# Kernel tuning notes

Measured on AMD Instinct MI355X. Metric: run time of the kernel, lower is better.

Reference implementation:

```python
import jax, jax.numpy as jnp
import numpy as np

Q_PTS = jnp.array([0.0, 0.25, 0.5, 0.75, 1.0], dtype=jnp.float32)
LN_EPS = 1e-5


def _lower_median(s):
    # torch.median returns the LOWER of the two middle values for even n
    return s[..., (s.shape[-1] - 1) // 2]


def _quantile_sorted(s, q):
    # torch.quantile default 'linear' interpolation, computed on pre-sorted s
    n = s.shape[-1]
    idx = q * (n - 1)
    lo = jnp.floor(idx).astype(jnp.int32)
    hi = jnp.ceil(idx).astype(jnp.int32)
    frac = (idx - lo).astype(s.dtype)
    return jnp.take(s, lo, axis=-1) * (1.0 - frac) + jnp.take(s, hi, axis=-1) * frac


def _robust_stats(flat):
    # flat: [L-1, B, N] -> [L-1, B, 7]  (median, MAD, 5 quantiles)
    s = jnp.sort(flat, axis=-1)
    med = _lower_median(s)[..., None]
    mad = _lower_median(jnp.sort(jnp.abs(flat - med), axis=-1))[..., None]
    q = _quantile_sorted(s, Q_PTS)
    return jnp.concatenate([med, mad, q], axis=-1)


def _layer_norm(x, eps=LN_EPS):
    mu = x.mean(-1, keepdims=True)
    var = ((x - mu) ** 2).mean(-1, keepdims=True)
    return (x - mu) * jax.lax.rsqrt(var + eps)


def _forward(ws, bs, fc1_w, fc1_b, ln_w, ln_b, gate_w, gate_b, fco_w, fco_b, scale):
    Lm1, B = ws.shape[0], ws.shape[1]
    w_flat = ws.reshape(Lm1, B, -1)
    b_flat = bs.reshape(Lm1, B, -1)
    w_feats = _robust_stats(w_flat)            # [L-1, B, 7]
    b_feats = _robust_stats(b_flat)            # [L-1, B, 7]
    g_mean = w_flat.mean(-1, keepdims=True)    # [L-1, B, 1]
    g_mad = jnp.zeros_like(g_mean)             # MAD over a size-1 axis is exactly 0
    combined = jnp.concatenate([w_feats, b_feats, g_mean, g_mad], axis=-1)  # [L-1, B, 16]
    x = _layer_norm(combined)                  # F.layer_norm without affine
    # ResidualMLP (vectorized over the layer axis l)
    h = jnp.einsum('lbi,lhi->lbh', x, fc1_w) + fc1_b[:, None, :]
    h = _layer_norm(h) * ln_w[:, None, :] + ln_b[:, None, :]
    h = jax.nn.gelu(h, approximate=False)      # nn.GELU() default = exact erf
    gate = jax.nn.sigmoid(jnp.einsum('lbh,lgh->lbg', h, gate_w) + gate_b[:, None, :])
    raw = jnp.einsum('lbg,log->lbo', h * gate, fco_w) + fco_b[:, None, :]
    return jnp.sin(raw) * scale[:, None, None] + 1.0   # [L-1, B, out_dim]


def setup_inputs() -> dict:
    key = jax.random.key(0)
    ks = jax.random.split(key, 8)
    Lm1, B, D, H, F_IN = 3, 64, 512, 64, 16
    return {
        'ws': jax.random.normal(ks[0], (Lm1, B, D, D), jnp.float32) * 0.05,
        'bs': jax.random.normal(ks[1], (Lm1, B, D), jnp.float32) * 0.05,
        'w_last': jax.random.normal(ks[2], (B, D, D), jnp.float32) * 0.05,
        'b_last': jax.random.normal(ks[3], (B, D), jnp.float32) * 0.05,
        'fc1_w': jax.random.normal(ks[4], (Lm1, H, F_IN), jnp.float32) * 0.2,
        'fc1_b': jnp.zeros((Lm1, H), jnp.float32),
        'ln_w': jnp.ones((Lm1, H), jnp.float32),
        'ln_b': jnp.zeros((Lm1, H), jnp.float32),
        'gate_w': jax.random.normal(ks[5], (Lm1, H, H), jnp.float32) * 0.15,
        'gate_b': jnp.zeros((Lm1, H), jnp.float32),
        'fco_w': jax.random.normal(ks[6], (Lm1, D, H), jnp.float32) * 0.1,
        'fco_b': jnp.zeros((Lm1, D), jnp.float32),
        'scale': jnp.full((Lm1,), 0.1, jnp.float32),
    }


def reference(ws, bs, w_last, b_last, fc1_w, fc1_b, ln_w, ln_b, gate_w, gate_b, fco_w, fco_b, scale):
    # w_last / b_last correspond to wsfeat[L-1]: received by forward but never used
    # (loop breaks at i == L-1), matching the torch module exactly.
    return _forward(ws, bs, fc1_w, fc1_b, ln_w, ln_b, gate_w, gate_b, fco_w, fco_b, scale)
```

## Files before the change

### kernel.cpp

```cpp
#include <hip/hip_runtime.h>
#include <cstdint>

#define NROW 192
#define NW   262144
#define NT   1024
#define QCAP 1024
#define SEGS_CAP 12288

__device__ __forceinline__ uint32_t mono(float x) {
    uint32_t u = __float_as_uint(x);
    return (u & 0x80000000u) ? ~u : (u | 0x80000000u);
}
__device__ __forceinline__ float unmono(uint32_t u) {
    uint32_t v = (u & 0x80000000u) ? (u & 0x7FFFFFFFu) : ~u;
    return __uint_as_float(v);
}
__device__ __forceinline__ int binof(float x, float lo, float s) {
    float d = (x - lo) * s;
    d = fminf(fmaxf(d, 0.0f), 4095.0f);
    return (int)d;
}

__device__ void block_select(const uint32_t* hist, int nb, uint32_t rank,
                             uint32_t* sbuf, volatile uint32_t* out, int tid) {
    int per = (nb + NT - 1) / NT;
    int base = tid * per;
    uint32_t s = 0;
    for (int i = 0; i < per; ++i) { int idx = base + i; if (idx < nb) s += hist[idx]; }
    uint32_t p = s;
    int lane = tid & 63;
    #pragma unroll
    for (int off = 1; off < 64; off <<= 1) {
        uint32_t v = __shfl_up(p, off);
        if (lane >= off) p += v;
    }
    int w = tid >> 6;
    if (lane == 63) sbuf[w] = p;
    __syncthreads();
    if (tid == 0) {
        uint32_t acc = 0;
        for (int i = 0; i < 16; ++i) { uint32_t t = sbuf[i]; sbuf[16 + i] = acc; acc += t; }
    }
    __syncthreads();
    uint32_t excl = sbuf[16 + w] + p - s;
    if (rank >= excl && rank < excl + s) {
        uint32_t rem = rank - excl;
        for (int i = 0; i < per; ++i) {
            int idx = base + i;
            if (idx >= nb) break;
            uint32_t c = hist[idx];
            if (rem < c) { out[0] = (uint32_t)idx; out[1] = rem; break; }
            rem -= c;
        }
    }
    __syncthreads();
}

__device__ uint32_t seg_select(const uint32_t* seg, uint32_t cnt, uint32_t rank,
                               uint32_t* hist2, uint32_t* sbuf,
                               volatile uint32_t* out2, int tid) {
    for (int i = tid; i < 2048; i += NT) hist2[i] = 0;
    __syncthreads();
    for (uint32_t i = tid; i < cnt; i += NT) atomicAdd(&hist2[seg[i] >> 21], 1u);
    __syncthreads();
    block_select(hist2, 2048, rank, sbuf, out2, tid);
    uint32_t b1 = out2[0], r1 = out2[1];
    __syncthreads();
    for (int i = tid; i < 2048; i += NT) hist2[i] = 0;
    __syncthreads();
    for (uint32_t i = tid; i < cnt; i += NT) {
        uint32_t k = seg[i];
        if ((k >> 21) == b1) atomicAdd(&hist2[(k >> 10) & 2047u], 1u);
    }
    __syncthreads();
    block_select(hist2, 2048, r1, sbuf, out2, tid);
    uint32_t b2 = out2[0], r2 = out2[1];
    __syncthreads();
    for (int i = tid; i < 1024; i += NT) hist2[i] = 0;
    __syncthreads();
    for (uint32_t i = tid; i < cnt; i += NT) {
        uint32_t k = seg[i];
        if ((k >> 21) == b1 && ((k >> 10) & 2047u) == b2)
            atomicAdd(&hist2[k & 1023u], 1u);
    }
    __syncthreads();
    block_select(hist2, 1024, r2, sbuf, out2, tid);
    uint32_t b3 = out2[0];
    __syncthreads();
    return (b1 << 21) + (b2 << 10) + b3;
}

__device__ uint32_t refine_global(const float4* p4, float med, int mode,
                                  uint32_t b1, uint32_t rem,
                                  uint32_t* hist2, uint32_t* sbuf,
                                  volatile uint32_t* out2, int tid) {
    for (int i = tid; i < 2048; i += NT) hist2[i] = 0;
    __syncthreads();
    for (int it = 0; it < 64; ++it) {
        float4 v = p4[tid + it * NT];
        float xs[4] = {v.x, v.y, v.z, v.w};
        #pragma unroll
        for (int c = 0; c < 4; ++c) {
            uint32_t u = mode ? __float_as_uint(fabsf(xs[c] - med)) : mono(xs[c]);
            if ((u >> 20) == b1) atomicAdd(&hist2[(u >> 9) & 2047u], 1u);
        }
    }
    __syncthreads();
    block_select(hist2, 2048, rem, sbuf, out2, tid);
    uint32_t b2 = out2[0], r2 = out2[1];
    __syncthreads();
    for (int i = tid; i < 512; i += NT) hist2[i] = 0;
    __syncthreads();
    for (int it = 0; it < 64; ++it) {
        float4 v = p4[tid + it * NT];
        float xs[4] = {v.x, v.y, v.z, v.w};
        #pragma unroll
        for (int c = 0; c < 4; ++c) {
            uint32_t u = mode ? __float_as_uint(fabsf(xs[c] - med)) : mono(xs[c]);
            if ((u >> 20) == b1 && ((u >> 9) & 2047u) == b2)
                atomicAdd(&hist2[u & 511u], 1u);
        }
    }
    __syncthreads();
    block_select(hist2, 512, r2, sbuf, out2, tid);
    uint32_t b3 = out2[0];
    __syncthreads();
    return (b1 << 20) + (b2 << 9) + b3;
}

__device__ void fb_path(const float4* p4, float* xf,
                        uint32_t* hist, uint32_t* hist2, uint32_t* sbuf,
                        volatile uint32_t* out2, int tid) {
    const uint32_t RANK6[6] = {65535u, 65536u, 131071u, 131072u, 196607u, 196608u};
    for (int i = tid; i < 4096; i += NT) hist[i] = 0;
    __syncthreads();
    for (int it = 0; it < 64; ++it) {
        float4 v = p4[tid + it * NT];
        float xs[4] = {v.x, v.y, v.z, v.w};
        #pragma unroll
        for (int c = 0; c < 4; ++c) atomicAdd(&hist[mono(xs[c]) >> 20], 1u);
    }
    __syncthreads();
    uint32_t bins[6], rems[6];
    for (int k = 0; k < 6; ++k) {
        block_select(hist, 4096, RANK6[k], sbuf, out2, tid);
        bins[k] = out2[0]; rems[k] = out2[1];
        __syncthreads();
    }
    float svv[6];
    for (int k = 0; k < 6; ++k)
        svv[k] = unmono(refine_global(p4, 0.f, 0, bins[k], rems[k], hist2, sbuf, out2, tid));
    if (tid == 0) {
        xf[0] = svv[2];
        xf[3] = 0.25f * svv[0] + 0.75f * svv[1];
        xf[4] = 0.5f  * (svv[2] + svv[3]);
        xf[5] = 0.75f * svv[4] + 0.25f * svv[5];
    }
    float med = svv[2];
    __syncthreads();
    for (int i = tid; i < 4096; i += NT) hist[i] = 0;
    __syncthreads();
    for (int it = 0; it < 64; ++it) {
        float4 v = p4[tid + it * NT];
        float xs[4] = {v.x, v.y, v.z, v.w};
        #pragma unroll
        for (int c = 0; c < 4; ++c)
            atomicAdd(&hist[__float_as_uint(fabsf(xs[c] - med)) >> 20], 1u);
    }
    __syncthreads();
    block_select(hist, 4096, 131071u, sbuf, out2, tid);
    uint32_t mb = out2[0], mr = out2[1];
    __syncthreads();
    uint32_t mu = refine_global(p4, med, 1, mb, mr, hist2, sbuf, out2, tid);
    if (tid == 0) xf[1] = __uint_as_float(mu);
}

__device__ __forceinline__ uint32_t Pv(const uint32_t* P, int k) {
    return (k >= 4096) ? (uint32_t)NW : P[k];
}
__device__ __forceinline__ uint32_t wup(float mL, float mR, float tau,
                                        float blo, float bsc, const uint32_t* P) {
    const int bR = binof(mR + tau, blo, bsc);
    const int bL = binof(mL - tau, blo, bsc);
    return Pv(P, bR + 1) - P[bL];
}
__device__ __forceinline__ uint32_t wlow(float mL, float mR, float tau,
                                         float blo, float bsc, const uint32_t* P) {
    const int bR = binof(mL + tau, blo, bsc);
    const int bL = binof(mR - tau, blo, bsc);
    const uint32_t a = P[bR];
    const uint32_t b = Pv(P, bL + 1);
    return (a > b) ? (a - b) : 0u;
}

__device__ void bitonic512w(float* a, int tid) {
    for (int k = 2; k <= 512; k <<= 1) {
        for (int j = k >> 1; j > 0; j >>= 1) {
            __syncthreads();
            if (tid < 512) {
                int i = tid, ixj = i ^ j;
                if (ixj > i) {
                    float x = a[i], y = a[ixj];
                    bool up = ((i & k) == 0);
                    if ((x > y) == up) { a[i] = y; a[ixj] = x; }
                }
            }
        }
    }
    __syncthreads();
}

__device__ void wstats_body(const float4* __restrict__ p4, float* xf,
                            uint32_t* hist, uint32_t* histB,
                            uint32_t* sbuf, uint32_t* segs,
                            uint32_t* ctrl, float* fctrl, int tid) {
    const int lane = tid & 63, wv = tid >> 6;
    float* fsb = (float*)sbuf;
    volatile uint32_t* out2 = (volatile uint32_t*)(ctrl + 62);

    {
        float smin = 1e30f, smax = -1e30f;
        #pragma unroll
        for (int k = 0; k < 8; ++k) {
            float4 v = p4[tid + k * NT];
            smin = fminf(smin, fminf(fminf(v.x, v.y), fminf(v.z, v.w)));
            smax = fmaxf(smax, fmaxf(fmaxf(v.x, v.y), fmaxf(v.z, v.w)));
        }
        #pragma unroll
        for (int off = 32; off > 0; off >>= 1) {
            smin = fminf(smin, __shfl_down(smin, off));
            smax = fmaxf(smax, __shfl_down(smax, off));
        }
        if (lane == 0) { fsb[wv * 2] = smin; fsb[wv * 2 + 1] = smax; }
        __syncthreads();
        if (tid == 0) {
            float mn = 1e30f, mx = -1e30f;
            for (int i = 0; i < 16; ++i) { mn = fminf(mn, fsb[i * 2]); mx = fmaxf(mx, fsb[i * 2 + 1]); }
            float span = mx - mn;
            float lo = mn - 0.0625f * span;
            float s = (span > 0.f) ? 4096.0f / (span * 1.125f) : 0.0f;
            fctrl[0] = lo; fctrl[1] = s;
        }
        __syncthreads();
    }
    const float blo = fctrl[0], bsc = fctrl[1];

    for (int i = tid; i < 4096; i += NT) { hist[i] = 0; histB[i] = 0; }
    __syncthreads();
    {
        uint32_t* hsel = (wv & 1) ? histB : hist;
        float sum = 0.f, fmn = 1e30f, fmx = -1e30f;
        for (int it = 0; it < 64; it += 8) {
            float4 a8[8];
            #pragma unroll
            for (int j = 0; j < 8; ++j) a8[j] = p4[tid + (it + j) * NT];
            #pragma unroll
            for (int j = 0; j < 8; ++j) {
                float xs[4] = {a8[j].x, a8[j].y, a8[j].z, a8[j].w};
                #pragma unroll
                for (int c = 0; c < 4; ++c) {
                    float x = xs[c];
                    sum += x;
                    fmn = fminf(fmn, x);
                    fmx = fmaxf(fmx, x);
                    atomicAdd(&hsel[binof(x, blo, bsc)], 1u);
                }
            }
        }
        #pragma unroll
        for (int off = 32; off > 0; off >>= 1) {
            sum += __shfl_down(sum, off);
            fmn = fminf(fmn, __shfl_down(fmn, off));
            fmx = fmaxf(fmx, __shfl_down(fmx, off));
        }
        __syncthreads();
        if (lane == 0) { fsb[wv * 4] = sum; fsb[wv * 4 + 1] = fmn; fsb[wv * 4 + 2] = fmx; }
        __syncthreads();
        if (tid == 0) { float s = 0; for (int i = 0; i < 16; ++i) s += fsb[i * 4]; xf[14] = s * (1.0f / (float)NW); }
        if (tid == 1) { float m = 1e30f;  for (int i = 0; i < 16; ++i) m = fminf(m, fsb[i * 4 + 1]); xf[2] = m; fctrl[2] = m; }
        if (tid == 2) { float M = -1e30f; for (int i = 0; i < 16; ++i) M = fmaxf(M, fsb[i * 4 + 2]); xf[6] = M; fctrl[3] = M; }
        if (tid == 3) xf[15] = 0.0f;
        __syncthreads();
        for (int i = tid; i < 4096; i += NT) hist[i] += histB[i];
        __syncthreads();
    }

    {
        const int b4 = tid * 4;
        const uint32_t v0 = hist[b4], v1 = hist[b4 + 1], v2 = hist[b4 + 2], v3 = hist[b4 + 3];
        const uint32_t s = v0 + v1 + v2 + v3;
        uint32_t p = s;
        #pragma unroll
        for (int off = 1; off < 64; off <<= 1) {
            uint32_t t = __shfl_up(p, off);
            if (lane >= off) p += t;
        }
        if (lane == 63) sbuf[wv] = p;
        __syncthreads();
        if (tid == 0) {
            uint32_t acc = 0;
            for (int i = 0; i < 16; ++i) { uint32_t t = sbuf[i]; sbuf[16 + i] = acc; acc += t; }
        }
        __syncthreads();
        const uint32_t excl = sbuf[16 + wv] + p - s;
        uint32_t ppA[5];
        ppA[0] = excl; ppA[1] = excl + v0; ppA[2] = ppA[1] + v1; ppA[3] = ppA[2] + v2; ppA[4] = ppA[3] + v3;
        hist[b4] = ppA[0]; hist[b4 + 1] = ppA[1]; hist[b4 + 2] = ppA[2]; hist[b4 + 3] = ppA[3];
        const uint32_t RANKS[6] = {65535u, 65536u, 131071u, 131072u, 196607u, 196608u};
        #pragma unroll
        for (int c = 0; c < 4; ++c) {
            #pragma unroll
            for (int q = 0; q < 6; ++q) {
                const uint32_t r = RANKS[q];
                if (ppA[c] <= r && r < ppA[c + 1]) {
                    ctrl[12 + q] = (uint32_t)(b4 + c);
                    ctrl[18 + q] = r - ppA[c];
                    ctrl[48 + q] = ppA[c + 1] - ppA[c];
                }
            }
        }
        __syncthreads();
    }

    if (tid == 0) {
        uint32_t ndl = 0, fail = 0;
        #pragma unroll
        for (int q = 0; q < 6; ++q) {
            const uint32_t b = ctrl[12 + q];
            int jf = -1;
            for (uint32_t t = 0; t < ndl; ++t) if (ctrl[24 + t] == b) { jf = (int)t; break; }
            if (jf < 0) {
                jf = (int)ndl;
                ctrl[24 + ndl] = b;
                ctrl[30 + ndl] = ctrl[48 + q];
                ndl++;
            }
            ctrl[36 + q] = (uint32_t)jf;
        }
        uint32_t off = 0;
        for (uint32_t t = 0; t < ndl; ++t) {
            ctrl[54 + t] = off;
            if (ctrl[30 + t] > QCAP) fail = 1;
            off += ctrl[30 + t];
        }
        if (off > 6144u) fail = 1;
        if (ctrl[14] == 0u || ctrl[14] == 4095u) fail = 1;
        ctrl[60] = off;
        ctrl[10] = ndl;
        ctrl[11] = fail;
        #pragma unroll
        for (int j = 0; j < 6; ++j) ctrl[j] = 0;
        ctrl[6] = 0;
        ctrl[7] = 0;
        ctrl[8] = 0;
        ctrl[9] = 0;
        ctrl[48] = 0xFFFFFFFFu; ctrl[49] = 0xFFFFFFFFu;
    }
    __syncthreads();
    if (ctrl[11]) { fb_path(p4, xf, hist, segs, sbuf, out2, tid); return; }

    const float wbin = 1.0f / bsc;
    const uint32_t m0 = ctrl[14];

    sbuf[tid] = 0;
    {
        const float mLf = blo + (float)m0 * wbin;
        const float mRf = mLf + wbin;
        #pragma unroll
        for (int c = 0; c < 4; ++c) {
            const int j = tid * 4 + c;
            const float tau = (float)j * wbin;
            const uint32_t up_j = wup(mLf, mRf, tau, blo, bsc, hist);
            if (up_j <= 131071u) {
                bool bnd = (j == 4095);
                if (!bnd) bnd = (wup(mLf, mRf, (float)(j + 1) * wbin, blo, bsc, hist) > 131071u);
                if (bnd) ctrl[48] = (uint32_t)j;
            }
            const uint32_t lo_j = wlow(mLf, mRf, tau, blo, bsc, hist);
            if (lo_j >= 131072u) {
                bool bnd = (j == 0);
                if (!bnd) bnd = (wlow(mLf, mRf, (float)(j - 1) * wbin, blo, bsc, hist) < 131072u);
                if (bnd) ctrl[49] = (uint32_t)j;
            }
        }
    }
    __syncthreads();
    if (tid < (int)ctrl[10]) ((uint8_t*)sbuf)[ctrl[24 + tid]] = (uint8_t)(tid + 1);
    const uint32_t jlo = ctrl[48], jhi = ctrl[49];
    float Awin = -1.0f;
    if (jlo != 0xFFFFFFFFu && jlo >= 2u) Awin = (float)(jlo - 2u) * wbin;
    float Bwin = (jhi == 0xFFFFFFFFu) ? 3.0e38f : (float)(jhi + 3u) * wbin;
    Bwin = fmaxf(Bwin, Awin + 3.0f * wbin);
    const float mtld = blo + ((float)m0 + 0.5f) * wbin;
    const uint32_t madbase = ctrl[60];
    __syncthreads();

    uint32_t myclo = 0;
    {
        const uint8_t* tbl = (const uint8_t*)sbuf;
        for (int it = 0; it < 64; it += 8) {
            float4 a8[8];
            #pragma unroll
            for (int j = 0; j < 8; ++j) a8[j] = p4[tid + (it + j) * NT];
            #pragma unroll
            for (int j = 0; j < 8; ++j) {
                float xs[4] = {a8[j].x, a8[j].y, a8[j].z, a8[j].w};
                #pragma unroll
                for (int c = 0; c < 4; ++c) {
                    float x = xs[c];
                    uint32_t m = tbl[binof(x, blo, bsc)];
                    if (m) {
                        uint32_t jj = m - 1u;
                        uint32_t pos = atomicAdd(&ctrl[jj], 1u);
                        if (pos < ctrl[30 + jj]) segs[ctrl[54 + jj] + pos] = mono(x);
                    }
                    float u = fabsf(x - mtld);
                    if (u <= Awin) myclo++;
                    else if (u <= Bwin) {
                        uint32_t pos = atomicAdd(&ctrl[6], 1u);
                        uint32_t slot = madbase + pos;
                        if (slot < SEGS_CAP) segs[slot] = __float_as_uint(x);
                    }
                }
            }
        }
    }
    __syncthreads();
    #pragma unroll
    for (int off = 32; off > 0; off >>= 1) myclo += __shfl_down(myclo, off);
    if (lane == 0) sbuf[wv] = myclo;
    __syncthreads();
    if (tid == 0) {
        uint32_t clo = 0;
        for (int i = 0; i < 16; ++i) clo += sbuf[i];
        ctrl[7] = clo;
        uint32_t fail = 0;
        const uint32_t ndl = ctrl[10];
        for (uint32_t j = 0; j < ndl; ++j) if (ctrl[j] != ctrl[30 + j]) fail = 1;
        if (ctrl[6] > SEGS_CAP - madbase) fail = 1;
        ctrl[11] = fail;
    }
    __syncthreads();
    if (ctrl[11]) { fb_path(p4, xf, hist, segs, sbuf, out2, tid); return; }

    {
        const uint32_t ndl = ctrl[10];
        for (uint32_t j = 0; j < ndl; ++j) {
            const uint32_t cnt = ctrl[j];
            const uint32_t base = ctrl[54 + j];
            if ((uint32_t)tid < cnt) {
                const uint32_t key = segs[base + tid];
                uint32_t r = 0;
                for (uint32_t i = 0; i < cnt; ++i) {
                    const uint32_t ki = segs[base + i];
                    r += (ki < key || (ki == key && i < (uint32_t)tid)) ? 1u : 0u;
                }
                #pragma unroll
                for (int q = 0; q < 6; ++q)
                    if (ctrl[36 + q] == j && ctrl[18 + q] == r) ctrl[42 + q] = key;
            }
        }
    }
    __syncthreads();
    const float med = unmono(ctrl[44]);
    if (tid == 0) {
        xf[0] = med;
        xf[3] = 0.25f * unmono(ctrl[42]) + 0.75f * unmono(ctrl[43]);
        xf[4] = 0.5f  * (med + unmono(ctrl[45]));
        xf[5] = 0.75f * unmono(ctrl[46]) + 0.25f * unmono(ctrl[47]);
    }

    const uint32_t mcnt = ctrl[6];
    const float thq = Awin + wbin;
    const float tcq = Bwin - 2.0f * wbin;
    uint32_t n2t = 0, n2c = 0;
    for (uint32_t i = (uint32_t)tid; i < mcnt; i += NT) {
        float x = __uint_as_float(segs[madbase + i]);
        float t = fabsf(x - med);
        segs[madbase + i] = __float_as_uint(t);
        n2t += (t <= thq) ? 1u : 0u;
        n2c += (t <= tcq) ? 1u : 0u;
    }
    #pragma unroll
    for (int off = 32; off > 0; off >>= 1) {
        n2t += __shfl_down(n2t, off);
        n2c += __shfl_down(n2c, off);
    }
    if (lane == 0) { atomicAdd(&ctrl[8], n2t); atomicAdd(&ctrl[9], n2c); }
    __syncthreads();
    if (tid == 0) {
        const uint32_t clo = ctrl[7];
        uint32_t fail = 0;
        if (clo > 131071u) fail = 1;
        if (clo + ctrl[8] > 131071u) fail = 1;
        if (clo + ctrl[9] < 131072u) fail = 1;
        if (!fail && (131071u - clo) >= mcnt) fail = 1;
        ctrl[11] = fail;
    }
    __syncthreads();
    if (ctrl[11]) { fb_path(p4, xf, hist, segs, sbuf, out2, tid); return; }
    const uint32_t kR = 131071u - ctrl[7];
    uint32_t madu = seg_select(segs + madbase, mcnt, kR, hist, sbuf, out2, tid);
    if (tid == 0) xf[1] = __uint_as_float(madu);
}

__global__ __launch_bounds__(NT) void fused_kernel(
    const float* __restrict__ wsrc, const float* __restrict__ bsrc,
    const float* __restrict__ fc1_w, const float* __restrict__ fc1_b,
    const float* __restrict__ ln_w,  const float* __restrict__ ln_b,
    const float* __restrict__ gate_w, const float* __restrict__ gate_b,
    const float* __restrict__ fco_w,  const float* __restrict__ fco_b,
    const float* __restrict__ scale,  float* __restrict__ out) {
    const int row = blockIdx.x;
    const int tid = threadIdx.x;
    const int l = row >> 6;
    __shared__ uint32_t hist[4096];
    __shared__ uint32_t histB[4096];
    __shared__ uint32_t sbuf[1024];
    __shared__ uint32_t segs[SEGS_CAP];
    __shared__ uint32_t ctrl[64];
    __shared__ float fctrl[8];
    __shared__ float xf[16], hm[64], hg[64], st2[2];

    {
        float* a = (float*)segs;
        float* d = ((float*)segs) + 512;
        const float* p = bsrc + (size_t)row * 512;
        if (tid < 512) a[tid] = p[tid];
        bitonic512w(a, tid);
        const float bmed = a[255];
        if (tid == 0) {
            xf[7]  = bmed;
            xf[9]  = a[0];
            xf[10] = 0.25f * a[127] + 0.75f * a[128];
            xf[11] = 0.5f  * (a[255] + a[256]);
            xf[12] = 0.75f * a[383] + 0.25f * a[384];
            xf[13] = a[511];
        }
        __syncthreads();
        if (tid < 512) d[tid] = fabsf(a[tid] - bmed);
        bitonic512w(d, tid);
        if (tid == 0) xf[8] = d[255];
        __syncthreads();
    }

    wstats_body((const float4*)(wsrc + (size_t)row * NW), xf,
                hist, histB, sbuf, segs, ctrl, fctrl, tid);
    __syncthreads();

    if (tid == 0) {
        float mu = 0.f;
        for (int i = 0; i < 16; ++i) mu += xf[i];
        mu *= (1.f / 16.f);
        float var = 0.f;
        for (int i = 0; i < 16; ++i) { float dd = xf[i] - mu; var += dd * dd; }
        var *= (1.f / 16.f);
        st2[0] = mu; st2[1] = rsqrtf(var + 1e-5f);
    }
    __syncthreads();
    if (tid < 16) xf[tid] = (xf[tid] - st2[0]) * st2[1];
    __syncthreads();
    if (tid < 64) {
        const float* wv = fc1_w + ((size_t)l * 64 + tid) * 16;
        float acc = fc1_b[l * 64 + tid];
        #pragma unroll
        for (int i = 0; i < 16; ++i) acc += xf[i] * wv[i];
        hm[tid] = acc;
    }
    __syncthreads();
    if (tid == 0) {
        float mu = 0.f;
        for (int i = 0; i < 64; ++i) mu += hm[i];
        mu *= (1.f / 64.f);
        float var = 0.f;
        for (int i = 0; i < 64; ++i) { float dd = hm[i] - mu; var += dd * dd; }
        var *= (1.f / 64.f);
        st2[0] = mu; st2[1] = rsqrtf(var + 1e-5f);
    }
    __syncthreads();
    if (tid < 64) {
        float v = (hm[tid] - st2[0]) * st2[1] * ln_w[l * 64 + tid] + ln_b[l * 64 + tid];
        hm[tid] = 0.5f * v * (1.0f + erff(v * 0.70710678118654752f));
    }
    __syncthreads();
    if (tid < 64) {
        const float* wv = gate_w + ((size_t)l * 64 + tid) * 64;
        float acc = gate_b[l * 64 + tid];
        #pragma unroll
        for (int i = 0; i < 64; ++i) acc += hm[i] * wv[i];
        float g = 1.0f / (1.0f + expf(-acc));
        hg[tid] = hm[tid] * g;
    }
    __syncthreads();
    const float sc = scale[l];
    for (int o = tid; o < 512; o += NT) {
        const float* wv = fco_w + ((size_t)l * 512 + o) * 64;
        float acc = fco_b[l * 512 + o];
        #pragma unroll
        for (int i = 0; i < 64; ++i) acc += hg[i] * wv[i];
        out[(size_t)row * 512 + o] = sinf(acc) * sc + 1.0f;
    }
}

extern "C" void kernel_launch(void* const* d_in, const int* in_sizes, int n_in,
                              void* d_out, int out_size, void* d_ws, size_t ws_size,
                              hipStream_t stream) {
    const float* ws_in  = (const float*)d_in[0];
    const float* bs_in  = (const float*)d_in[1];
    const float* fc1_w  = (const float*)d_in[4];
    const float* fc1_b  = (const float*)d_in[5];
    const float* ln_w   = (const float*)d_in[6];
    const float* ln_b   = (const float*)d_in[7];
    const float* gate_w = (const float*)d_in[8];
    const float* gate_b = (const float*)d_in[9];
    const float* fco_w  = (const float*)d_in[10];
    const float* fco_b  = (const float*)d_in[11];
    const float* scale  = (const float*)d_in[12];
    float* out  = (float*)d_out;

    hipLaunchKernelGGL(fused_kernel, dim3(NROW), dim3(NT), 0, stream,
                       ws_in, bs_in, fc1_w, fc1_b, ln_w, ln_b, gate_w, gate_b,
                       fco_w, fco_b, scale, out);
}
```

Measured before the change: 424.3 us.

## Sort bias rows in one wavefront's registers and use four histogram copies

The 512-element bias sort no longer uses a shared-memory bitonic network with a block-wide barrier per step. It now runs inside a single wavefront, holding the data in registers and exchanging values with shuffles, so the rest of the block starts the weight pass straight away. The histogram build spreads atomics over four shared histograms instead of two to cut contention, and both streaming passes load 16 float4 per batch instead of 8. The cost is more LDS (an extra 32KB, which may lower occupancy) and higher register pressure.

```diff
diff --git a/kernel.cpp b/kernel.cpp
--- a/kernel.cpp
+++ b/kernel.cpp
@@ -193,25 +193,44 @@
     return (a > b) ? (a - b) : 0u;
 }
 
-__device__ void bitonic512w(float* a, int tid) {
-    for (int k = 2; k <= 512; k <<= 1) {
-        for (int j = k >> 1; j > 0; j >>= 1) {
-            __syncthreads();
-            if (tid < 512) {
-                int i = tid, ixj = i ^ j;
-                if (ixj > i) {
-                    float x = a[i], y = a[ixj];
-                    bool up = ((i & k) == 0);
-                    if ((x > y) == up) { a[i] = y; a[ixj] = x; }
+__device__ __forceinline__ void regsort512(float v[8], int lane) {
+    #pragma unroll
+    for (int kk = 1; kk <= 9; ++kk) {
+        const int k = 1 << kk;
+        #pragma unroll
+        for (int jj = kk - 1; jj >= 0; --jj) {
+            const int j = 1 << jj;
+            if (j >= 64) {
+                const int jr = j >> 6;
+                const int kr = k >> 6;
+                #pragma unroll
+                for (int r = 0; r < 8; ++r) {
+                    if ((r & jr) == 0) {
+                        const bool up = ((r & kr) == 0);
+                        float x = v[r], y = v[r | jr];
+                        float mn = fminf(x, y), mx = fmaxf(x, y);
+                        v[r]      = up ? mn : mx;
+                        v[r | jr] = up ? mx : mn;
+                    }
                 }
-            }
-        }
-    }
-    __syncthreads();
+            } else {
+                #pragma unroll
+                for (int r = 0; r < 8; ++r) {
+                    const int i = (r << 6) | lane;
+                    const bool up = ((i & k) == 0);
+                    const bool lower = ((lane & j) == 0);
+                    float x = v[r];
+                    float y = __shfl_xor(x, j);
+                    v[r] = (lower == up) ? fminf(x, y) : fmaxf(x, y);
+                }
+            }
+        }
+    }
 }
 
 __device__ void wstats_body(const float4* __restrict__ p4, float* xf,
                             uint32_t* hist, uint32_t* histB,
+                            uint32_t* histC, uint32_t* histD,
                             uint32_t* sbuf, uint32_t* segs,
                             uint32_t* ctrl, float* fctrl, int tid) {
     const int lane = tid & 63, wv = tid >> 6;
@@ -245,17 +264,18 @@
     }
     const float blo = fctrl[0], bsc = fctrl[1];
 
-    for (int i = tid; i < 4096; i += NT) { hist[i] = 0; histB[i] = 0; }
+    for (int i = tid; i < 4096; i += NT) { hist[i] = 0; histB[i] = 0; histC[i] = 0; histD[i] = 0; }
     __syncthreads();
     {
-        uint32_t* hsel = (wv & 1) ? histB : hist;
+        const int hs = wv & 3;
+        uint32_t* hsel = (hs == 0) ? hist : ((hs == 1) ? histB : ((hs == 2) ? histC : histD));
         float sum = 0.f, fmn = 1e30f, fmx = -1e30f;
-        for (int it = 0; it < 64; it += 8) {
-            float4 a8[8];
+        for (int it = 0; it < 64; it += 16) {
+            float4 a8[16];
             #pragma unroll
-            for (int j = 0; j < 8; ++j) a8[j] = p4[tid + (it + j) * NT];
+            for (int j = 0; j < 16; ++j) a8[j] = p4[tid + (it + j) * NT];
             #pragma unroll
-            for (int j = 0; j < 8; ++j) {
+            for (int j = 0; j < 16; ++j) {
                 float xs[4] = {a8[j].x, a8[j].y, a8[j].z, a8[j].w};
                 #pragma unroll
                 for (int c = 0; c < 4; ++c) {
@@ -281,7 +301,7 @@
         if (tid == 2) { float M = -1e30f; for (int i = 0; i < 16; ++i) M = fmaxf(M, fsb[i * 4 + 2]); xf[6] = M; fctrl[3] = M; }
         if (tid == 3) xf[15] = 0.0f;
         __syncthreads();
-        for (int i = tid; i < 4096; i += NT) hist[i] += histB[i];
+        for (int i = tid; i < 4096; i += NT) hist[i] += histB[i] + histC[i] + histD[i];
         __syncthreads();
     }
 
@@ -398,12 +418,12 @@
     uint32_t myclo = 0;
     {
         const uint8_t* tbl = (const uint8_t*)sbuf;
-        for (int it = 0; it < 64; it += 8) {
-            float4 a8[8];
+        for (int it = 0; it < 64; it += 16) {
+            float4 a8[16];
             #pragma unroll
-            for (int j = 0; j < 8; ++j) a8[j] = p4[tid + (it + j) * NT];
+            for (int j = 0; j < 16; ++j) a8[j] = p4[tid + (it + j) * NT];
             #pragma unroll
-            for (int j = 0; j < 8; ++j) {
+            for (int j = 0; j < 16; ++j) {
                 float xs[4] = {a8[j].x, a8[j].y, a8[j].z, a8[j].w};
                 #pragma unroll
                 for (int c = 0; c < 4; ++c) {
@@ -516,36 +536,48 @@
     const int l = row >> 6;
     __shared__ uint32_t hist[4096];
     __shared__ uint32_t histB[4096];
+    __shared__ uint32_t histC[4096];
+    __shared__ uint32_t histD[4096];
     __shared__ uint32_t sbuf[1024];
     __shared__ uint32_t segs[SEGS_CAP];
     __shared__ uint32_t ctrl[64];
     __shared__ float fctrl[8];
     __shared__ float xf[16], hm[64], hg[64], st2[2];
 
-    {
-        float* a = (float*)segs;
-        float* d = ((float*)segs) + 512;
+    if (tid < 64) {
+        const int lane = tid;
         const float* p = bsrc + (size_t)row * 512;
-        if (tid < 512) a[tid] = p[tid];
-        bitonic512w(a, tid);
-        const float bmed = a[255];
-        if (tid == 0) {
+        float v[8];
+        #pragma unroll
+        for (int r = 0; r < 8; ++r) v[r] = p[(r << 6) | lane];
+        regsort512(v, lane);
+        const float a0   = __shfl(v[0], 0);
+        const float a127 = __shfl(v[1], 63);
+        const float a128 = __shfl(v[2], 0);
+        const float a255 = __shfl(v[3], 63);
+        const float a256 = __shfl(v[4], 0);
+        const float a383 = __shfl(v[5], 63);
+        const float a384 = __shfl(v[6], 0);
+        const float a511 = __shfl(v[7], 63);
+        const float bmed = a255;
+        float t[8];
+        #pragma unroll
+        for (int r = 0; r < 8; ++r) t[r] = fabsf(v[r] - bmed);
+        regsort512(t, lane);
+        const float d255 = __shfl(t[3], 63);
+        if (lane == 0) {
             xf[7]  = bmed;
-            xf[9]  = a[0];
-            xf[10] = 0.25f * a[127] + 0.75f * a[128];
-            xf[11] = 0.5f  * (a[255] + a[256]);
-            xf[12] = 0.75f * a[383] + 0.25f * a[384];
-            xf[13] = a[511];
-        }
-        __syncthreads();
-        if (tid < 512) d[tid] = fabsf(a[tid] - bmed);
-        bitonic512w(d, tid);
-        if (tid == 0) xf[8] = d[255];
-        __syncthreads();
+            xf[8]  = d255;
+            xf[9]  = a0;
+            xf[10] = 0.25f * a127 + 0.75f * a128;
+            xf[11] = 0.5f  * (a255 + a256);
+            xf[12] = 0.75f * a383 + 0.25f * a384;
+            xf[13] = a511;
+        }
     }
 
     wstats_body((const float4*)(wsrc + (size_t)row * NW), xf,
-                hist, histB, sbuf, segs, ctrl, fctrl, tid);
+                hist, histB, histC, histD, sbuf, segs, ctrl, fctrl, tid);
     __syncthreads();
 
     if (tid == 0) {
```

Result: no change. 420.4 us (-0.9%).
